# Optimization experiments

Hardware: AMD Instinct MI355X
Metric: run time of the kernel (lower is better)

The kernel has to match this reference:

```python
import jax, jax.numpy as jnp
import numpy as np

EMBED_DIM = 1024
ATTN_DIM = 1024


def setup_inputs() -> dict:
    key = jax.random.key(0)
    k1, k2, k3, k4 = jax.random.split(key, 4)
    scale = 1.0 / np.sqrt(EMBED_DIM)
    return {
        "embedded": jax.random.normal(k1, (4, 2048, EMBED_DIM), dtype=jnp.float32),
        # weights stored as [in, out] (torch Linear applies x @ W.T)
        "Wk": jax.random.uniform(k2, (EMBED_DIM, ATTN_DIM), dtype=jnp.float32, minval=-scale, maxval=scale),
        "Wq": jax.random.uniform(k3, (EMBED_DIM, ATTN_DIM), dtype=jnp.float32, minval=-scale, maxval=scale),
        "Wv": jax.random.uniform(k4, (EMBED_DIM, ATTN_DIM), dtype=jnp.float32, minval=-scale, maxval=scale),
    }


def reference(embedded, Wk, Wq, Wv):
    b, t, _ = embedded.shape
    k = embedded @ Wk  # [b, t, d]
    q = embedded @ Wq
    v = embedded @ Wv
    scores = jnp.einsum("btd,bsd->bts", q, k) / jnp.sqrt(jnp.float32(k.shape[-1]))
    causal = jnp.tril(jnp.ones((t, t), dtype=bool))  # [t, t]
    scores = jnp.where(causal, scores, -jnp.inf)
    w = jax.nn.softmax(scores, axis=-1)
    o = jnp.einsum("bts,bsd->btd", w, v)
    return jnp.round(o * 10000.0) / 10000.0
```

## Files before the change

### kernel.cpp

```cpp
#include <hip/hip_runtime.h>
#include <cmath>

typedef _Float16 half8 __attribute__((ext_vector_type(8)));
typedef _Float16 half4 __attribute__((ext_vector_type(4)));
typedef float floatx4 __attribute__((ext_vector_type(4)));

__device__ __forceinline__ void load_lds16(const void* g, void* l) {
  __builtin_amdgcn_global_load_lds((const __attribute__((address_space(1))) void*)g,
                                   (__attribute__((address_space(3))) void*)l, 16, 0, 0);
}

__device__ __forceinline__ unsigned lds_addr(const void* p) {
  return (unsigned)(unsigned long long)(const __attribute__((address_space(3))) void*)p;
}

__device__ __forceinline__ half8 ds_read128(unsigned addr) {
  half8 r;
  asm volatile("ds_read_b128 %0, %1" : "=v"(r) : "v"(addr));
  return r;
}


__global__ void prep_kernel(const float* __restrict__ emb, const float* __restrict__ Wq,
                            const float* __restrict__ Wk, const float* __restrict__ Wv,
                            _Float16* __restrict__ Xp, _Float16* __restrict__ Wqp,
                            _Float16* __restrict__ Wkp, _Float16* __restrict__ Wvtp) {
  int p = blockIdx.x;
  if (p < 640) {
    __shared__ _Float16 lds[16 * 1032];
    const float* src;
    _Float16* dst;
    if (p < 512)      { src = emb + (size_t)p * 16384;        dst = Xp  + (size_t)p * 16384; }
    else if (p < 576) { src = Wq + (size_t)(p - 512) * 16384; dst = Wqp + (size_t)(p - 512) * 16384; }
    else              { src = Wk + (size_t)(p - 576) * 16384; dst = Wkp + (size_t)(p - 576) * 16384; }
    for (int it = 0; it < 16; ++it) {
      int idx = it * 256 + threadIdx.x;
      int row = idx >> 8, c4 = idx & 255;
      float4 v = ((const float4*)src)[row * 256 + c4];
      half4 h;
      h[0] = (_Float16)v.x; h[1] = (_Float16)v.y; h[2] = (_Float16)v.z; h[3] = (_Float16)v.w;
      *(half4*)(lds + row * 1032 + c4 * 4) = h;
    }
    __syncthreads();
    for (int it = 0; it < 8; ++it) {
      int c = it * 256 + threadIdx.x;
      int kb = c >> 6, k16 = (c >> 4) & 3, r = c & 15;
      half8 h = *(const half8*)(lds + r * 1032 + kb * 32 + k16 * 8);
      *(half8*)(dst + (size_t)c * 8) = h;
    }
  } else {
    __shared__ float tile[32][33];
    int q = p - 640;
    int n0 = (q & 31) * 32, k0 = (q >> 5) * 32;
    int c = threadIdx.x & 31, r8 = threadIdx.x >> 5;
    for (int pp = 0; pp < 4; ++pp) {
      int r = pp * 8 + r8;
      tile[r][c] = Wv[(size_t)(k0 + r) * 1024 + n0 + c];
    }
    __syncthreads();
    if (threadIdx.x < 128) {
      int rr = threadIdx.x & 31;
      int k16 = (threadIdx.x >> 5) & 3;
      half8 h;
      for (int kk = 0; kk < 8; ++kk) h[kk] = (_Float16)tile[k16 * 8 + kk][rr];
      int n_row = n0 + rr;
      size_t chunk = ((size_t)(n_row >> 4) * 32 + (k0 >> 5)) * 64 + (k16 << 4) + (n_row & 15);
      *(half8*)(Wvtp + chunk * 8) = h;
    }
  }
}

__device__ __forceinline__ void gemm_core(const _Float16* __restrict__ Ap, int kbA, int tA0,
                                          const _Float16* __restrict__ Bp, int kbB, int tB0,
                                          int kIters, _Float16* sA, _Float16* sB,
                                          floatx4 acc[4][4]) {
  int tid = threadIdx.x;
  int lane = tid & 63, wave = tid >> 6;
  int wm = (wave >> 1) << 6, wn = (wave & 1) << 6;
  const _Float16* gA0 = Ap + ((size_t)(tA0 + 2 * wave) * kbA) * 512 + lane * 8;
  const _Float16* gA1 = Ap + ((size_t)(tA0 + 2 * wave + 1) * kbA) * 512 + lane * 8;
  const _Float16* gB0 = Bp + ((size_t)(tB0 + 2 * wave) * kbB) * 512 + lane * 8;
  const _Float16* gB1 = Bp + ((size_t)(tB0 + 2 * wave + 1) * kbB) * 512 + lane * 8;
  int ta = wm >> 4, tb = wn >> 4, lo = lane * 8;
  int wo = wave * 1024;

  load_lds16(gA0, sA + wo);
  load_lds16(gA1, sA + wo + 512);
  load_lds16(gB0, sB + wo);
  load_lds16(gB1, sB + wo + 512);
  __syncthreads();

  int cur = 0;
  for (int kt = 0; kt < kIters; ++kt) {
    if (kt + 1 < kIters) {
      size_t kb = (size_t)(kt + 1) * 512;
      int nx = (cur ^ 1) << 12;
      load_lds16(gA0 + kb, sA + nx + wo);
      load_lds16(gA1 + kb, sA + nx + wo + 512);
      load_lds16(gB0 + kb, sB + nx + wo);
      load_lds16(gB1 + kb, sB + nx + wo + 512);
    }
    const _Float16* cA = sA + (cur << 12);
    const _Float16* cB = sB + (cur << 12);
    half8 af[4], bf[4];
    for (int i = 0; i < 4; ++i) af[i] = *(const half8*)(cA + (ta + i) * 512 + lo);
    for (int j = 0; j < 4; ++j) bf[j] = *(const half8*)(cB + (tb + j) * 512 + lo);
    __builtin_amdgcn_s_setprio(1);
    for (int i = 0; i < 4; ++i)
      for (int j = 0; j < 4; ++j)
        acc[i][j] = __builtin_amdgcn_mfma_f32_16x16x32_f16(af[i], bf[j], acc[i][j], 0, 0, 0);
    __builtin_amdgcn_s_setprio(0);
    if (kt + 1 < kIters) {
      __syncthreads();
      cur ^= 1;
    }
  }
}

__global__ void mt_kernel(const _Float16* __restrict__ Wkp, const _Float16* __restrict__ Wqp,
                          _Float16* __restrict__ Mtp) {
  __shared__ __align__(16) _Float16 sA[8192];
  __shared__ __align__(16) _Float16 sB[8192];
  floatx4 acc[4][4];
  for (int i = 0; i < 4; ++i)
    for (int j = 0; j < 4; ++j) acc[i][j] = (floatx4){0.f, 0.f, 0.f, 0.f};
  int m0 = blockIdx.y * 128, n0 = blockIdx.x * 128;
  gemm_core(Wkp, 32, m0 >> 4, Wqp, 32, n0 >> 4, 32, sA, sB, acc);
  int lane = threadIdx.x & 63, wave = threadIdx.x >> 6;
  int wm = (wave >> 1) << 6, wn = (wave & 1) << 6;
  int quad = lane >> 4, cl = lane & 15;
  for (int i = 0; i < 4; ++i)
    for (int j = 0; j < 4; ++j)
      for (int rr = 0; rr < 4; ++rr) {
        int row = m0 + wm + i * 16 + quad * 4 + rr;
        int col = n0 + wn + j * 16 + cl;
        size_t chunk = ((size_t)(row >> 4) * 32 + (col >> 5)) * 64 + (((col >> 3) & 3) << 4) + (row & 15);
        Mtp[chunk * 8 + (col & 7)] = (_Float16)acc[i][j][rr];
      }
}

#define NT_PROJ 16

__global__ __launch_bounds__(512, 2) void proj256_kernel(
    const _Float16* __restrict__ Ap, const _Float16* __restrict__ Bp,
    _Float16* __restrict__ XMp, _Float16* __restrict__ Vtp) {
  __shared__ __align__(16) _Float16 sh[65536];
  int tid = threadIdx.x;
  int lane = tid & 63, w = tid >> 6;
  int wr = w >> 2, wc = w & 3;
  int orig = blockIdx.x;
  int tile = (orig & 7) * 32 + (orig >> 3);
  int mtile = tile >> 3, ntile = tile & 7;
  int tA0 = mtile * 16, tB0 = ntile * 16;

  const _Float16* gB[4];
  int ldsB[4];
  for (int i = 0; i < 4; ++i) {
    int cb = w * 4 + i, pc = cb >> 1, kb = cb & 1;
    gB[i] = Bp + ((size_t)(tB0 + pc) * 32 + kb) * 512 + lane * 8;
    ldsB[i] = 16384 + cb * 512;
  }
  const _Float16* gA[4];
  int ldsA[4];
  {
    int kbw = w & 1, pihi = (w >> 2) * 8, pilo = (w >> 1) & 1;
    for (int q = 0; q < 4; ++q) {
      int p = 2 * q + pilo + pihi;
      gA[q] = Ap + ((size_t)(tA0 + p) * 32 + kbw) * 512 + lane * 8;
      ldsA[q] = (p * 2 + kbw) * 512;
    }
  }

  unsigned L = lds_addr(sh);
  unsigned baseA = L + (unsigned)(wr * 16384 + lane * 16);
  unsigned baseB = L + 32768u + (unsigned)(wc * 8192 + lane * 16);

  floatx4 acc[8][4];
  for (int m = 0; m < 8; ++m)
    for (int n = 0; n < 4; ++n) acc[m][n] = (floatx4){0.f, 0.f, 0.f, 0.f};

  for (int tt = 0; tt < 2; ++tt) {
    int bo = tt << 15;
    for (int i = 0; i < 4; ++i) load_lds16(gB[i] + (size_t)tt * 1024, sh + bo + ldsB[i]);
    for (int q = 0; q < 4; ++q) load_lds16(gA[q] + (size_t)tt * 1024, sh + bo + ldsA[q]);
  }
  asm volatile("s_waitcnt vmcnt(8)" ::: "memory");
  __builtin_amdgcn_s_barrier();

  half8 bf[4][2];
#pragma unroll 2
  for (int t = 0; t < NT_PROJ; ++t) {
    int bo = (t & 1) << 15;
    unsigned bob = (unsigned)(t & 1) << 16;
    unsigned aA = baseA + bob, aB = baseB + bob;
#pragma unroll
    for (int q = 0; q < 4; ++q) {
      half8 af[2][2];
      if (q == 0) {
        for (int n = 0; n < 4; ++n)
          for (int kb = 0; kb < 2; ++kb)
            bf[n][kb] = ds_read128(aB + (unsigned)(n * 2048 + kb * 1024));
      }
      for (int mm = 0; mm < 2; ++mm)
        for (int kb = 0; kb < 2; ++kb)
          af[mm][kb] = ds_read128(aA + (unsigned)((2 * q + mm) * 2048 + kb * 1024));
      if (q == 0) {
        if (t >= 1 && t + 1 < NT_PROJ)
          load_lds16(gA[3] + (size_t)(t + 1) * 1024, sh + (bo ^ 32768) + ldsA[3]);
      } else if (q == 1) {
        if (t + 2 < NT_PROJ)
          for (int i = 0; i < 4; ++i)
            load_lds16(gB[i] + (size_t)(t + 2) * 1024, sh + bo + ldsB[i]);
      } else if (q == 2) {
        if (t + 2 < NT_PROJ) {
          load_lds16(gA[0] + (size_t)(t + 2) * 1024, sh + bo + ldsA[0]);
          load_lds16(gA[1] + (size_t)(t + 2) * 1024, sh + bo + ldsA[1]);
        }
      } else {
        if (t < NT_PROJ - 1) {
          if (t + 2 < NT_PROJ) asm volatile("s_waitcnt vmcnt(6)" ::: "memory");
          else                 asm volatile("s_waitcnt vmcnt(0)" ::: "memory");
        }
        if (t + 2 < NT_PROJ)
          load_lds16(gA[2] + (size_t)(t + 2) * 1024, sh + bo + ldsA[2]);
      }
      __builtin_amdgcn_s_barrier();
      asm volatile("s_waitcnt lgkmcnt(0)" ::: "memory");
      __builtin_amdgcn_sched_barrier(0);
      __builtin_amdgcn_s_setprio(1);
      for (int mm = 0; mm < 2; ++mm)
        for (int n = 0; n < 4; ++n)
          for (int kb = 0; kb < 2; ++kb)
            acc[2 * q + mm][n] =
                __builtin_amdgcn_mfma_f32_16x16x32_f16(af[mm][kb], bf[n][kb], acc[2 * q + mm][n], 0, 0, 0);
      __builtin_amdgcn_s_setprio(0);
      __builtin_amdgcn_sched_barrier(0);
      __builtin_amdgcn_s_barrier();
    }
  }

  int quad = lane >> 4, cl = lane & 15;
  int which = ntile >> 2;
  for (int m = 0; m < 8; ++m)
    for (int n = 0; n < 4; ++n)
      for (int rr = 0; rr < 4; ++rr) {
        int rl = wr * 128 + m * 16 + quad * 4 + rr;
        int cg = wc * 64 + n * 16 + cl;
        _Float16 val = (_Float16)acc[m][n][rr];
        int lh;
        if (which) {
          lh = (((cg >> 4) * 8 + (rl >> 5)) << 9) + (((rl >> 3) & 3) << 7) + ((cg & 15) << 3) + (rl & 7);
        } else {
          lh = (((rl >> 4) * 8 + (cg >> 5)) << 9) + (((cg >> 3) & 3) << 7) + ((rl & 15) << 3) + (cg & 7);
        }
        sh[lh] = val;
      }
  __syncthreads();
  int b = mtile >> 3;
  if (which) {
    _Float16* dst = Vtp + (size_t)b * 2097152;
    for (int p = 0; p < 16; ++p) {
      size_t GB = (((size_t)(ntile & 3) * 16 + p) * 64 + (mtile & 7) * 8) * 512;
      *(half8*)(dst + GB + tid * 8) = *(const half8*)(sh + p * 4096 + tid * 8);
    }
  } else {
    _Float16* dst = XMp + (size_t)b * 2097152;
    for (int p = 0; p < 16; ++p) {
      size_t GB = (((size_t)(mtile & 7) * 16 + p) * 32 + (ntile & 3) * 8) * 512;
      *(half8*)(dst + GB + tid * 8) = *(const half8*)(sh + p * 4096 + tid * 8);
    }
  }
}

__global__ void qke_kernel(const _Float16* __restrict__ XMp, const _Float16* __restrict__ Xp,
                           _Float16* __restrict__ E, float* __restrict__ lsum) {
  __shared__ __align__(16) _Float16 sh[16384];
  int x = blockIdx.x, b = blockIdx.y;
  int p = (x & 7) * 17 + (x >> 3);
  int ti = 0;
  while ((ti + 1) * (ti + 2) / 2 <= p) ++ti;
  int tj = p - ti * (ti + 1) / 2;
  const _Float16* Ab = XMp + (size_t)b * 2097152;
  const _Float16* Bb = Xp + (size_t)b * 2097152;
  _Float16* Eb = E + (size_t)b * 4194304;
  floatx4 acc[4][4];
  for (int i = 0; i < 4; ++i)
    for (int j = 0; j < 4; ++j) acc[i][j] = (floatx4){0.f, 0.f, 0.f, 0.f};
  gemm_core(Ab, 32, ti * 8, Bb, 32, tj * 8, 32, sh, sh + 8192, acc);
  int lane = threadIdx.x & 63, wave = threadIdx.x >> 6;
  int wm = (wave >> 1) << 6, wn = (wave & 1) << 6;
  int quad = lane >> 4, cl = lane & 15;
  float rs[4][4];
  for (int i = 0; i < 4; ++i)
    for (int rr = 0; rr < 4; ++rr) rs[i][rr] = 0.f;
  __syncthreads();
  for (int i = 0; i < 4; ++i)
    for (int j = 0; j < 4; ++j)
      for (int rr = 0; rr < 4; ++rr) {
        int rl = wm + i * 16 + quad * 4 + rr;
        int cg = wn + j * 16 + cl;
        int row = ti * 128 + rl, col = tj * 128 + cg;
        float e = 0.f;
        if (col <= row) e = __expf(acc[i][j][rr] * 0.03125f - 12.0f);
        _Float16 eh = (_Float16)e;
        rs[i][rr] += (float)eh;
        int lh = (((rl >> 4) * 4 + (cg >> 5)) << 9) + (((cg >> 3) & 3) << 7) + ((rl & 15) << 3) + (cg & 7);
        sh[lh] = eh;
      }
  __syncthreads();
  for (int pp = 0; pp < 8; ++pp) {
    size_t GB = ((size_t)(ti * 8 + pp) * 64 + tj * 4) * 512;
    *(half8*)(Eb + GB + threadIdx.x * 8) = *(const half8*)(sh + pp * 2048 + threadIdx.x * 8);
  }
  float* lb = lsum + (size_t)b * 2048;
  for (int i = 0; i < 4; ++i)
    for (int rr = 0; rr < 4; ++rr) {
      float v = rs[i][rr];
      v += __shfl_xor(v, 1, 64);
      v += __shfl_xor(v, 2, 64);
      v += __shfl_xor(v, 4, 64);
      v += __shfl_xor(v, 8, 64);
      if (cl == 0) atomicAdd(lb + ti * 128 + wm + i * 16 + quad * 4 + rr, v);
    }
}

__global__ void pv_kernel(const _Float16* __restrict__ E, const _Float16* __restrict__ Vtp,
                          const float* __restrict__ lsum, float* __restrict__ out) {
  __shared__ __align__(16) _Float16 sA[8192];
  __shared__ __align__(16) _Float16 sB[8192];
  int orig = blockIdx.x + 8 * (blockIdx.y + 16 * blockIdx.z);
  int logical = (orig & 7) * 64 + (orig >> 3);
  int n0 = (logical & 7) * 128;
  int rest = logical >> 3;
  int y = rest & 15, b = rest >> 4;
  int ti = (y & 1) ? (15 - (y >> 1)) : (y >> 1);
  const _Float16* Pb = E + (size_t)b * 4194304;
  const _Float16* Vb = Vtp + (size_t)b * 2097152;
  floatx4 acc[4][4];
  for (int i = 0; i < 4; ++i)
    for (int j = 0; j < 4; ++j) acc[i][j] = (floatx4){0.f, 0.f, 0.f, 0.f};
  gemm_core(Vb, 64, n0 >> 4, Pb, 64, ti * 8, (ti + 1) * 4, sA, sB, acc);
  int lane = threadIdx.x & 63, wave = threadIdx.x >> 6;
  int wm = (wave >> 1) << 6, wn = (wave & 1) << 6;
  int quad = lane >> 4, cl = lane & 15;
  const float* lb = lsum + (size_t)b * 2048;
  for (int j = 0; j < 4; ++j) {
    int t = ti * 128 + wn + j * 16 + cl;
    float inv = 1.0f / lb[t];
    float* orow = out + ((size_t)b * 2048 + t) * 1024;
    for (int i = 0; i < 4; ++i) {
      int d0 = n0 + wm + i * 16 + quad * 4;
      float4 v;
      v.x = rintf(acc[i][j][0] * inv * 10000.f) * 1e-4f;
      v.y = rintf(acc[i][j][1] * inv * 10000.f) * 1e-4f;
      v.z = rintf(acc[i][j][2] * inv * 10000.f) * 1e-4f;
      v.w = rintf(acc[i][j][3] * inv * 10000.f) * 1e-4f;
      *(float4*)(orow + d0) = v;
    }
  }
}

extern "C" void kernel_launch(void* const* d_in, const int* in_sizes, int n_in,
                              void* d_out, int out_size, void* d_ws, size_t ws_size,
                              hipStream_t stream) {
  const float* emb = (const float*)d_in[0];
  const float* Wk = (const float*)d_in[1];
  const float* Wq = (const float*)d_in[2];
  const float* Wv = (const float*)d_in[3];
  float* out = (float*)d_out;

  _Float16* ws = (_Float16*)d_ws;
  _Float16* Xp   = ws;
  _Float16* Wqp  = Xp + (size_t)8192 * 1024;
  _Float16* Wkp  = Wqp + (size_t)1024 * 1024;
  _Float16* Mtp  = Wkp + (size_t)1024 * 1024;
  _Float16* Wvtp = Mtp + (size_t)1024 * 1024;
  _Float16* XMp  = Wvtp + (size_t)1024 * 1024;
  _Float16* Vtp  = XMp + (size_t)8192 * 1024;
  _Float16* Ebuf = Vtp + (size_t)8192 * 1024;
  float* lsum    = (float*)(Ebuf + (size_t)16 * 1024 * 1024);

  hipMemsetAsync(lsum, 0, 4 * 2048 * sizeof(float), stream);
  prep_kernel<<<1664, 256, 0, stream>>>(emb, Wq, Wk, Wv, Xp, Wqp, Wkp, Wvtp);
  mt_kernel<<<dim3(8, 8), 256, 0, stream>>>(Wkp, Wqp, Mtp);
  proj256_kernel<<<256, 512, 0, stream>>>(Xp, Mtp, XMp, Vtp);
  qke_kernel<<<dim3(136, 4), 256, 0, stream>>>(XMp, Xp, Ebuf, lsum);
  pv_kernel<<<dim3(8, 16, 4), 256, 0, stream>>>(Ebuf, Vtp, lsum, out);
}
```

Baseline: 225.5 us.

## Split PV kernel K-loop across two wave groups with LDS reduction

The PV GEMM block grows from 256 to 512 threads, and each 256-thread group computes half of the causal K range into its own LDS buffers. The second group then writes its partial accumulators to shared memory, and the first group adds them before normalising and storing. This aims to shorten the long serial K loop for late row tiles and to raise the number of waves per CU. The cost is double the LDS per block, an extra exchange through shared memory, and added register pressure under the 512-thread launch bound.

```diff
diff --git a/kernel.cpp b/kernel.cpp
--- a/kernel.cpp
+++ b/kernel.cpp
@@ -70,17 +70,16 @@
   }
 }
 
-__device__ __forceinline__ void gemm_core(const _Float16* __restrict__ Ap, int kbA, int tA0,
-                                          const _Float16* __restrict__ Bp, int kbB, int tB0,
-                                          int kIters, _Float16* sA, _Float16* sB,
-                                          floatx4 acc[4][4]) {
-  int tid = threadIdx.x;
-  int lane = tid & 63, wave = tid >> 6;
+__device__ __forceinline__ void gemm_core_g(int lane, int wave,
+                                            const _Float16* __restrict__ Ap, int kbA, int tA0,
+                                            const _Float16* __restrict__ Bp, int kbB, int tB0,
+                                            int kb0, int kIters, _Float16* sA, _Float16* sB,
+                                            floatx4 acc[4][4]) {
   int wm = (wave >> 1) << 6, wn = (wave & 1) << 6;
-  const _Float16* gA0 = Ap + ((size_t)(tA0 + 2 * wave) * kbA) * 512 + lane * 8;
-  const _Float16* gA1 = Ap + ((size_t)(tA0 + 2 * wave + 1) * kbA) * 512 + lane * 8;
-  const _Float16* gB0 = Bp + ((size_t)(tB0 + 2 * wave) * kbB) * 512 + lane * 8;
-  const _Float16* gB1 = Bp + ((size_t)(tB0 + 2 * wave + 1) * kbB) * 512 + lane * 8;
+  const _Float16* gA0 = Ap + ((size_t)(tA0 + 2 * wave) * kbA + kb0) * 512 + lane * 8;
+  const _Float16* gA1 = Ap + ((size_t)(tA0 + 2 * wave + 1) * kbA + kb0) * 512 + lane * 8;
+  const _Float16* gB0 = Bp + ((size_t)(tB0 + 2 * wave) * kbB + kb0) * 512 + lane * 8;
+  const _Float16* gB1 = Bp + ((size_t)(tB0 + 2 * wave + 1) * kbB + kb0) * 512 + lane * 8;
   int ta = wm >> 4, tb = wn >> 4, lo = lane * 8;
   int wo = wave * 1024;
 
@@ -115,6 +114,13 @@
       cur ^= 1;
     }
   }
+}
+
+__device__ __forceinline__ void gemm_core(const _Float16* __restrict__ Ap, int kbA, int tA0,
+                                          const _Float16* __restrict__ Bp, int kbB, int tB0,
+                                          int kIters, _Float16* sA, _Float16* sB,
+                                          floatx4 acc[4][4]) {
+  gemm_core_g(threadIdx.x & 63, threadIdx.x >> 6, Ap, kbA, tA0, Bp, kbB, tB0, 0, kIters, sA, sB, acc);
 }
 
 __global__ void mt_kernel(const _Float16* __restrict__ Wkp, const _Float16* __restrict__ Wqp,
@@ -324,10 +330,10 @@
     }
 }
 
-__global__ void pv_kernel(const _Float16* __restrict__ E, const _Float16* __restrict__ Vtp,
-                          const float* __restrict__ lsum, float* __restrict__ out) {
-  __shared__ __align__(16) _Float16 sA[8192];
-  __shared__ __align__(16) _Float16 sB[8192];
+__global__ __launch_bounds__(512, 4) void pv_kernel(
+    const _Float16* __restrict__ E, const _Float16* __restrict__ Vtp,
+    const float* __restrict__ lsum, float* __restrict__ out) {
+  __shared__ __align__(16) _Float16 sh2[32768];
   int orig = blockIdx.x + 8 * (blockIdx.y + 16 * blockIdx.z);
   int logical = (orig & 7) * 64 + (orig >> 3);
   int n0 = (logical & 7) * 128;
@@ -336,26 +342,41 @@
   int ti = (y & 1) ? (15 - (y >> 1)) : (y >> 1);
   const _Float16* Pb = E + (size_t)b * 4194304;
   const _Float16* Vb = Vtp + (size_t)b * 2097152;
+  int tid = threadIdx.x;
+  int g = tid >> 8, lane = tid & 63, wave = (tid >> 6) & 3;
+  int half = (ti + 1) * 2;
+  _Float16* sA = sh2 + g * 16384;
+  _Float16* sB = sA + 8192;
   floatx4 acc[4][4];
   for (int i = 0; i < 4; ++i)
     for (int j = 0; j < 4; ++j) acc[i][j] = (floatx4){0.f, 0.f, 0.f, 0.f};
-  gemm_core(Vb, 64, n0 >> 4, Pb, 64, ti * 8, (ti + 1) * 4, sA, sB, acc);
-  int lane = threadIdx.x & 63, wave = threadIdx.x >> 6;
-  int wm = (wave >> 1) << 6, wn = (wave & 1) << 6;
-  int quad = lane >> 4, cl = lane & 15;
-  const float* lb = lsum + (size_t)b * 2048;
-  for (int j = 0; j < 4; ++j) {
-    int t = ti * 128 + wn + j * 16 + cl;
-    float inv = 1.0f / lb[t];
-    float* orow = out + ((size_t)b * 2048 + t) * 1024;
-    for (int i = 0; i < 4; ++i) {
-      int d0 = n0 + wm + i * 16 + quad * 4;
-      float4 v;
-      v.x = rintf(acc[i][j][0] * inv * 10000.f) * 1e-4f;
-      v.y = rintf(acc[i][j][1] * inv * 10000.f) * 1e-4f;
-      v.z = rintf(acc[i][j][2] * inv * 10000.f) * 1e-4f;
-      v.w = rintf(acc[i][j][3] * inv * 10000.f) * 1e-4f;
-      *(float4*)(orow + d0) = v;
+  gemm_core_g(lane, wave, Vb, 64, n0 >> 4, Pb, 64, ti * 8, g * half, half, sA, sB, acc);
+  __syncthreads();
+  floatx4* xch = (floatx4*)sh2;
+  if (g == 1) {
+    for (int i = 0; i < 4; ++i)
+      for (int j = 0; j < 4; ++j) xch[(tid - 256) * 16 + i * 4 + j] = acc[i][j];
+  }
+  __syncthreads();
+  if (g == 0) {
+    int wm = (wave >> 1) << 6, wn = (wave & 1) << 6;
+    int quad = lane >> 4, cl = lane & 15;
+    const float* lb = lsum + (size_t)b * 2048;
+    for (int j = 0; j < 4; ++j) {
+      int t = ti * 128 + wn + j * 16 + cl;
+      float inv = 1.0f / lb[t];
+      float* orow = out + ((size_t)b * 2048 + t) * 1024;
+      for (int i = 0; i < 4; ++i) {
+        floatx4 a = acc[i][j];
+        floatx4 p = xch[tid * 16 + i * 4 + j];
+        int d0 = n0 + wm + i * 16 + quad * 4;
+        float4 v;
+        v.x = rintf((a[0] + p[0]) * inv * 10000.f) * 1e-4f;
+        v.y = rintf((a[1] + p[1]) * inv * 10000.f) * 1e-4f;
+        v.z = rintf((a[2] + p[2]) * inv * 10000.f) * 1e-4f;
+        v.w = rintf((a[3] + p[3]) * inv * 10000.f) * 1e-4f;
+        *(float4*)(orow + d0) = v;
+      }
     }
   }
 }
@@ -385,5 +406,5 @@
   mt_kernel<<<dim3(8, 8), 256, 0, stream>>>(Wkp, Wqp, Mtp);
   proj256_kernel<<<256, 512, 0, stream>>>(Xp, Mtp, XMp, Vtp);
   qke_kernel<<<dim3(136, 4), 256, 0, stream>>>(XMp, Xp, Ebuf, lsum);
-  pv_kernel<<<dim3(8, 16, 4), 256, 0, stream>>>(Ebuf, Vtp, lsum, out);
-}
+  pv_kernel<<<dim3(8, 16, 4), 512, 0, stream>>>(Ebuf, Vtp, lsum, out);
+}
```

Measured after the change: 219.3 us. -2.8%, faster.
